# Optimization experiments

Hardware: AMD Instinct MI355X
Metric: run time of the kernel (lower is better)

The kernel has to match this reference:

```python
import jax, jax.numpy as jnp
import numpy as np

EMBED_DIM = 1024
ATTN_DIM = 256
B, NQ, NK = 16, 1, 4096


def setup_inputs() -> dict:
    key = jax.random.key(0)
    ks = jax.random.split(key, 7)
    return {
        "q": jax.random.normal(ks[0], (B, NQ, EMBED_DIM), dtype=jnp.float32),
        "k": jax.random.normal(ks[1], (B, NK, EMBED_DIM), dtype=jnp.float32),
        "v": jax.random.normal(ks[2], (B, NK, EMBED_DIM), dtype=jnp.float32),
        "W_kq": jax.random.normal(ks[3], (EMBED_DIM, ATTN_DIM), dtype=jnp.float32) * (1.0 / np.sqrt(EMBED_DIM)),
        "b_kq": jax.random.normal(ks[4], (ATTN_DIM,), dtype=jnp.float32) * 0.02,
        "W_v": jax.random.normal(ks[5], (EMBED_DIM, EMBED_DIM), dtype=jnp.float32) * (1.0 / np.sqrt(EMBED_DIM)),
        "b_v": jax.random.normal(ks[6], (EMBED_DIM,), dtype=jnp.float32) * 0.02,
    }


def reference(q, k, v, W_kq, b_kq, W_v, b_v):
    # Shared kq projection applied to both q and k (embedding_dim -> attention_dim)
    qp = jnp.einsum("bqd,da->bqa", q, W_kq) + b_kq          # [B, NQ, A]
    kp = jnp.einsum("bkd,da->bka", k, W_kq) + b_kq          # [B, NK, A]
    vp = jnp.einsum("bkd,de->bke", v, W_v) + b_v            # [B, NK, E]
    # scores = q @ k^T / sqrt(attention_dim)  (k.shape[2] after projection)
    scores = jnp.einsum("bqa,bka->bqk", qp, kp) / jnp.sqrt(
        jnp.asarray(kp.shape[2], dtype=qp.dtype))
    attn = jax.nn.softmax(scores, axis=2)                   # [B, NQ, NK]
    out = jnp.einsum("bqk,bke->bqe", attn, vp)              # [B, NQ, E]
    return out.squeeze(1)                                   # [B, E] since NQ == 1
```

## Files before the change

### kernel.cpp

```cpp
#include <hip/hip_runtime.h>

#define ED 1024
#define AD 256
#define BB 16
#define NK 4096
#define NCH 64
#define KCH (NK/NCH)

#define OFF_QP   0
#define OFF_T    4096
#define OFF_WSUM 20480
#define OFF_PART 21504
#define OFF_OV   1070080

__global__ void k_qp(const float* __restrict__ q, const float* __restrict__ Wkq,
                     const float* __restrict__ bkq, float* __restrict__ qp) {
    int b = blockIdx.x, cg = blockIdx.y, tid = threadIdx.x;
    int c = cg * 64 + (tid & 63), dg = tid >> 6;
    __shared__ float qsh[ED];
    ((float4*)qsh)[tid] = ((const float4*)(q + b * ED))[tid];
    __syncthreads();
    float acc = 0.f;
    #pragma unroll 8
    for (int d = dg; d < ED; d += 4) acc += qsh[d] * Wkq[(size_t)d * AD + c];
    __shared__ float red[4][64];
    red[dg][tid & 63] = acc;
    __syncthreads();
    if (tid < 64) {
        float s = red[0][tid] + red[1][tid] + red[2][tid] + red[3][tid];
        qp[b * AD + cg * 64 + tid] = s + bkq[cg * 64 + tid];
    }
}

__global__ void k_t(const float* __restrict__ Wkq, const float* __restrict__ qp,
                    float* __restrict__ t) {
    int b = blockIdx.y, dbase = blockIdx.x * 128;
    int tid = threadIdx.x, wave = tid >> 6, lane = tid & 63;
    float4 qv = ((const float4*)(qp + b * AD))[lane];
    for (int r = 0; r < 32; ++r) {
        int d = dbase + wave * 32 + r;
        float4 w = ((const float4*)(Wkq + (size_t)d * AD))[lane];
        float s = w.x * qv.x + w.y * qv.y + w.z * qv.z + w.w * qv.w;
        #pragma unroll
        for (int off = 32; off; off >>= 1) s += __shfl_down(s, off, 64);
        if (lane == 0) t[b * ED + d] = s;
    }
}

__global__ void k_fused(const float* __restrict__ k, const float* __restrict__ v,
                        const float* __restrict__ t, float* __restrict__ partial,
                        float* __restrict__ wsum) {
    int ch = blockIdx.x, b = blockIdx.y;
    int tid = threadIdx.x, wave = tid >> 6, lane = tid & 63;
    const float4* tb = (const float4*)(t + b * ED);
    float4 t0 = tb[lane], t1 = tb[64 + lane], t2 = tb[128 + lane], t3 = tb[192 + lane];
    __shared__ float ash[KCH];
    int row0 = ch * KCH + wave * 16;
    for (int r = 0; r < 16; ++r) {
        const float4* krow = (const float4*)(k + ((size_t)b * NK + row0 + r) * ED);
        float4 k0 = krow[lane], k1 = krow[64 + lane], k2 = krow[128 + lane], k3 = krow[192 + lane];
        float s = k0.x*t0.x + k0.y*t0.y + k0.z*t0.z + k0.w*t0.w
                + k1.x*t1.x + k1.y*t1.y + k1.z*t1.z + k1.w*t1.w
                + k2.x*t2.x + k2.y*t2.y + k2.z*t2.z + k2.w*t2.w
                + k3.x*t3.x + k3.y*t3.y + k3.z*t3.z + k3.w*t3.w;
        #pragma unroll
        for (int off = 32; off; off >>= 1) s += __shfl_down(s, off, 64);
        if (lane == 0) ash[wave * 16 + r] = __expf(s * 0.0625f);
    }
    __syncthreads();
    if (tid < KCH) {
        float s = ash[tid];
        #pragma unroll
        for (int off = 32; off; off >>= 1) s += __shfl_down(s, off, 64);
        if (tid == 0) wsum[b * NCH + ch] = s;
    }
    const float4* vb = (const float4*)(v + ((size_t)b * NK + (size_t)ch * KCH) * ED);
    float4 acc = {0.f, 0.f, 0.f, 0.f};
    #pragma unroll 4
    for (int kk = 0; kk < KCH; ++kk) {
        float wt = ash[kk];
        float4 vv = vb[(size_t)kk * (ED / 4) + tid];
        acc.x += wt * vv.x; acc.y += wt * vv.y; acc.z += wt * vv.z; acc.w += wt * vv.w;
    }
    ((float4*)partial)[((size_t)(b * NCH + ch)) * (ED / 4) + tid] = acc;
}

__global__ void k_reduce(const float* __restrict__ partial, const float* __restrict__ wsum,
                         float* __restrict__ ov) {
    int b = blockIdx.x, tid = threadIdx.x;
    __shared__ float lsh;
    if (tid < 64) {
        float s = wsum[b * NCH + tid];
        #pragma unroll
        for (int off = 32; off; off >>= 1) s += __shfl_down(s, off, 64);
        if (tid == 0) lsh = s;
    }
    __syncthreads();
    float linv = 1.0f / lsh;
    const float4* pb = (const float4*)(partial + (size_t)b * NCH * ED);
    float4 s4 = {0.f, 0.f, 0.f, 0.f};
    #pragma unroll 8
    for (int ch = 0; ch < NCH; ++ch) {
        float4 p = pb[(size_t)ch * (ED / 4) + tid];
        s4.x += p.x; s4.y += p.y; s4.z += p.z; s4.w += p.w;
    }
    s4.x *= linv; s4.y *= linv; s4.z *= linv; s4.w *= linv;
    ((float4*)(ov + b * ED))[tid] = s4;
}

__global__ void k_out(const float* __restrict__ ov, const float* __restrict__ Wv,
                      const float* __restrict__ bv, float* __restrict__ out) {
    int cb = blockIdx.x, tid = threadIdx.x;
    int col = cb * 64 + (tid & 63), dg = tid >> 6;
    __shared__ float ovsh[BB][ED];
    for (int i = tid; i < BB * ED / 4; i += 256)
        ((float4*)&ovsh[0][0])[i] = ((const float4*)ov)[i];
    __syncthreads();
    float acc[BB];
    #pragma unroll
    for (int b = 0; b < BB; ++b) acc[b] = 0.f;
    #pragma unroll 4
    for (int d = dg; d < ED; d += 4) {
        float w = Wv[(size_t)d * ED + col];
        #pragma unroll
        for (int b = 0; b < BB; ++b) acc[b] += ovsh[b][d] * w;
    }
    __shared__ float red[BB][256];
    #pragma unroll
    for (int b = 0; b < BB; ++b) red[b][tid] = acc[b];
    __syncthreads();
    #pragma unroll
    for (int bb = 0; bb < 4; ++bb) {
        int b = bb * 4 + (tid >> 6);
        int c = tid & 63;
        float s = red[b][c] + red[b][64 + c] + red[b][128 + c] + red[b][192 + c];
        out[b * ED + cb * 64 + c] = s + bv[cb * 64 + c];
    }
}

extern "C" void kernel_launch(void* const* d_in, const int* in_sizes, int n_in,
                              void* d_out, int out_size, void* d_ws, size_t ws_size,
                              hipStream_t stream) {
    const float* q   = (const float*)d_in[0];
    const float* k   = (const float*)d_in[1];
    const float* v   = (const float*)d_in[2];
    const float* Wkq = (const float*)d_in[3];
    const float* bkq = (const float*)d_in[4];
    const float* Wv  = (const float*)d_in[5];
    const float* bv  = (const float*)d_in[6];
    float* out = (float*)d_out;
    float* ws  = (float*)d_ws;

    float* qp      = ws + OFF_QP;
    float* t       = ws + OFF_T;
    float* wsum    = ws + OFF_WSUM;
    float* partial = ws + OFF_PART;
    float* ov      = ws + OFF_OV;

    k_qp    <<<dim3(16, 4),   256, 0, stream>>>(q, Wkq, bkq, qp);
    k_t     <<<dim3(8, 16),   256, 0, stream>>>(Wkq, qp, t);
    k_fused <<<dim3(NCH, BB), 256, 0, stream>>>(k, v, t, partial, wsum);
    k_reduce<<<16,            256, 0, stream>>>(partial, wsum, ov);
    k_out   <<<16,            256, 0, stream>>>(ov, Wv, bv, out);
}
```

Measured before the change: 208.4 us.

## Split reduce and output projection across more blocks, add final reduction kernel

Launches k_reduce and k_out on a 16x4 grid instead of 16 blocks, so each block handles one quarter of the embedding or reduction dimension. A new k_final kernel sums the four partial output projections and adds the bias. The change also processes two rows per iteration in k_t and k_fused for more memory-level parallelism, and raises the unroll factor of the V accumulation loop. The aim is to fill more compute units in the tail kernels, which were badly underoccupied. The cost is an extra kernel launch and an extra workspace round trip.

```diff
diff --git a/kernel.cpp b/kernel.cpp
--- a/kernel.cpp
+++ b/kernel.cpp
@@ -7,11 +7,12 @@
 #define NCH 64
 #define KCH (NK/NCH)
 
-#define OFF_QP   0
-#define OFF_T    4096
-#define OFF_WSUM 20480
-#define OFF_PART 21504
-#define OFF_OV   1070080
+#define OFF_QP    0
+#define OFF_T     4096
+#define OFF_WSUM  20480
+#define OFF_PART  21504
+#define OFF_OV    1070080
+#define OFF_OPART 1086464
 
 __global__ void k_qp(const float* __restrict__ q, const float* __restrict__ Wkq,
                      const float* __restrict__ bkq, float* __restrict__ qp) {
@@ -37,13 +38,19 @@
     int b = blockIdx.y, dbase = blockIdx.x * 128;
     int tid = threadIdx.x, wave = tid >> 6, lane = tid & 63;
     float4 qv = ((const float4*)(qp + b * AD))[lane];
-    for (int r = 0; r < 32; ++r) {
-        int d = dbase + wave * 32 + r;
-        float4 w = ((const float4*)(Wkq + (size_t)d * AD))[lane];
-        float s = w.x * qv.x + w.y * qv.y + w.z * qv.z + w.w * qv.w;
-        #pragma unroll
-        for (int off = 32; off; off >>= 1) s += __shfl_down(s, off, 64);
-        if (lane == 0) t[b * ED + d] = s;
+    for (int r = 0; r < 16; ++r) {
+        int d1 = dbase + wave * 32 + r;
+        int d2 = d1 + 16;
+        float4 w1 = ((const float4*)(Wkq + (size_t)d1 * AD))[lane];
+        float4 w2 = ((const float4*)(Wkq + (size_t)d2 * AD))[lane];
+        float s1 = w1.x*qv.x + w1.y*qv.y + w1.z*qv.z + w1.w*qv.w;
+        float s2 = w2.x*qv.x + w2.y*qv.y + w2.z*qv.z + w2.w*qv.w;
+        #pragma unroll
+        for (int off = 32; off; off >>= 1) {
+            s1 += __shfl_down(s1, off, 64);
+            s2 += __shfl_down(s2, off, 64);
+        }
+        if (lane == 0) { t[b * ED + d1] = s1; t[b * ED + d2] = s2; }
     }
 }
 
@@ -56,16 +63,28 @@
     float4 t0 = tb[lane], t1 = tb[64 + lane], t2 = tb[128 + lane], t3 = tb[192 + lane];
     __shared__ float ash[KCH];
     int row0 = ch * KCH + wave * 16;
-    for (int r = 0; r < 16; ++r) {
-        const float4* krow = (const float4*)(k + ((size_t)b * NK + row0 + r) * ED);
-        float4 k0 = krow[lane], k1 = krow[64 + lane], k2 = krow[128 + lane], k3 = krow[192 + lane];
-        float s = k0.x*t0.x + k0.y*t0.y + k0.z*t0.z + k0.w*t0.w
-                + k1.x*t1.x + k1.y*t1.y + k1.z*t1.z + k1.w*t1.w
-                + k2.x*t2.x + k2.y*t2.y + k2.z*t2.z + k2.w*t2.w
-                + k3.x*t3.x + k3.y*t3.y + k3.z*t3.z + k3.w*t3.w;
-        #pragma unroll
-        for (int off = 32; off; off >>= 1) s += __shfl_down(s, off, 64);
-        if (lane == 0) ash[wave * 16 + r] = __expf(s * 0.0625f);
+    for (int r = 0; r < 8; ++r) {
+        const float4* ka = (const float4*)(k + ((size_t)b * NK + row0 + r) * ED);
+        const float4* kb = (const float4*)(k + ((size_t)b * NK + row0 + r + 8) * ED);
+        float4 a0 = ka[lane], a1 = ka[64 + lane], a2 = ka[128 + lane], a3 = ka[192 + lane];
+        float4 b0 = kb[lane], b1 = kb[64 + lane], b2 = kb[128 + lane], b3 = kb[192 + lane];
+        float sa = a0.x*t0.x + a0.y*t0.y + a0.z*t0.z + a0.w*t0.w
+                 + a1.x*t1.x + a1.y*t1.y + a1.z*t1.z + a1.w*t1.w
+                 + a2.x*t2.x + a2.y*t2.y + a2.z*t2.z + a2.w*t2.w
+                 + a3.x*t3.x + a3.y*t3.y + a3.z*t3.z + a3.w*t3.w;
+        float sb = b0.x*t0.x + b0.y*t0.y + b0.z*t0.z + b0.w*t0.w
+                 + b1.x*t1.x + b1.y*t1.y + b1.z*t1.z + b1.w*t1.w
+                 + b2.x*t2.x + b2.y*t2.y + b2.z*t2.z + b2.w*t2.w
+                 + b3.x*t3.x + b3.y*t3.y + b3.z*t3.z + b3.w*t3.w;
+        #pragma unroll
+        for (int off = 32; off; off >>= 1) {
+            sa += __shfl_down(sa, off, 64);
+            sb += __shfl_down(sb, off, 64);
+        }
+        if (lane == 0) {
+            ash[wave * 16 + r]     = __expf(sa * 0.0625f);
+            ash[wave * 16 + r + 8] = __expf(sb * 0.0625f);
+        }
     }
     __syncthreads();
     if (tid < KCH) {
@@ -76,7 +95,7 @@
     }
     const float4* vb = (const float4*)(v + ((size_t)b * NK + (size_t)ch * KCH) * ED);
     float4 acc = {0.f, 0.f, 0.f, 0.f};
-    #pragma unroll 4
+    #pragma unroll 8
     for (int kk = 0; kk < KCH; ++kk) {
         float wt = ash[kk];
         float4 vv = vb[(size_t)kk * (ED / 4) + tid];
@@ -87,7 +106,8 @@
 
 __global__ void k_reduce(const float* __restrict__ partial, const float* __restrict__ wsum,
                          float* __restrict__ ov) {
-    int b = blockIdx.x, tid = threadIdx.x;
+    int b = blockIdx.x, dq = blockIdx.y, tid = threadIdx.x;
+    int chg = tid >> 6, c = tid & 63;
     __shared__ float lsh;
     if (tid < 64) {
         float s = wsum[b * NCH + tid];
@@ -95,47 +115,73 @@
         for (int off = 32; off; off >>= 1) s += __shfl_down(s, off, 64);
         if (tid == 0) lsh = s;
     }
-    __syncthreads();
-    float linv = 1.0f / lsh;
     const float4* pb = (const float4*)(partial + (size_t)b * NCH * ED);
     float4 s4 = {0.f, 0.f, 0.f, 0.f};
     #pragma unroll 8
-    for (int ch = 0; ch < NCH; ++ch) {
-        float4 p = pb[(size_t)ch * (ED / 4) + tid];
+    for (int ch = chg; ch < NCH; ch += 4) {
+        float4 p = pb[(size_t)ch * (ED / 4) + dq * 64 + c];
         s4.x += p.x; s4.y += p.y; s4.z += p.z; s4.w += p.w;
     }
-    s4.x *= linv; s4.y *= linv; s4.z *= linv; s4.w *= linv;
-    ((float4*)(ov + b * ED))[tid] = s4;
+    __shared__ float4 red[4][64];
+    red[chg][c] = s4;
+    __syncthreads();
+    if (tid < 64) {
+        float4 a0 = red[0][tid], a1 = red[1][tid], a2 = red[2][tid], a3 = red[3][tid];
+        float linv = 1.0f / lsh;
+        float4 r;
+        r.x = (a0.x + a1.x + a2.x + a3.x) * linv;
+        r.y = (a0.y + a1.y + a2.y + a3.y) * linv;
+        r.z = (a0.z + a1.z + a2.z + a3.z) * linv;
+        r.w = (a0.w + a1.w + a2.w + a3.w) * linv;
+        ((float4*)(ov + b * ED + dq * 256))[tid] = r;
+    }
 }
 
 __global__ void k_out(const float* __restrict__ ov, const float* __restrict__ Wv,
-                      const float* __restrict__ bv, float* __restrict__ out) {
-    int cb = blockIdx.x, tid = threadIdx.x;
+                      float* __restrict__ opart) {
+    int cb = blockIdx.x, dq = blockIdx.y, tid = threadIdx.x;
     int col = cb * 64 + (tid & 63), dg = tid >> 6;
-    __shared__ float ovsh[BB][ED];
-    for (int i = tid; i < BB * ED / 4; i += 256)
-        ((float4*)&ovsh[0][0])[i] = ((const float4*)ov)[i];
+    __shared__ float ovsh[BB][256];
+    for (int i = tid; i < BB * 64; i += 256) {
+        int bb = i >> 6, c4 = i & 63;
+        ((float4*)ovsh[bb])[c4] = ((const float4*)(ov + bb * ED + dq * 256))[c4];
+    }
     __syncthreads();
     float acc[BB];
     #pragma unroll
     for (int b = 0; b < BB; ++b) acc[b] = 0.f;
-    #pragma unroll 4
-    for (int d = dg; d < ED; d += 4) {
-        float w = Wv[(size_t)d * ED + col];
-        #pragma unroll
-        for (int b = 0; b < BB; ++b) acc[b] += ovsh[b][d] * w;
+    #pragma unroll 8
+    for (int it = 0; it < 64; ++it) {
+        int dd = dg + it * 4;
+        float w = Wv[(size_t)(dq * 256 + dd) * ED + col];
+        #pragma unroll
+        for (int b = 0; b < BB; ++b) acc[b] += ovsh[b][dd] * w;
     }
     __shared__ float red[BB][256];
     #pragma unroll
     for (int b = 0; b < BB; ++b) red[b][tid] = acc[b];
     __syncthreads();
-    #pragma unroll
-    for (int bb = 0; bb < 4; ++bb) {
-        int b = bb * 4 + (tid >> 6);
-        int c = tid & 63;
+    int bgrp = tid >> 6, c = tid & 63;
+    #pragma unroll
+    for (int bi = 0; bi < 4; ++bi) {
+        int b = bgrp * 4 + bi;
         float s = red[b][c] + red[b][64 + c] + red[b][128 + c] + red[b][192 + c];
-        out[b * ED + cb * 64 + c] = s + bv[cb * 64 + c];
-    }
+        opart[((size_t)(dq * BB + b)) * ED + cb * 64 + c] = s;
+    }
+}
+
+__global__ void k_final(const float* __restrict__ opart, const float* __restrict__ bv,
+                        float* __restrict__ out) {
+    int b = blockIdx.x, tid = threadIdx.x;
+    float4 s = ((const float4*)(opart + (size_t)(0 * BB + b) * ED))[tid];
+    #pragma unroll
+    for (int dq = 1; dq < 4; ++dq) {
+        float4 p = ((const float4*)(opart + (size_t)(dq * BB + b) * ED))[tid];
+        s.x += p.x; s.y += p.y; s.z += p.z; s.w += p.w;
+    }
+    float4 bb = ((const float4*)bv)[tid];
+    s.x += bb.x; s.y += bb.y; s.z += bb.z; s.w += bb.w;
+    ((float4*)(out + b * ED))[tid] = s;
 }
 
 extern "C" void kernel_launch(void* const* d_in, const int* in_sizes, int n_in,
@@ -156,10 +202,12 @@
     float* wsum    = ws + OFF_WSUM;
     float* partial = ws + OFF_PART;
     float* ov      = ws + OFF_OV;
+    float* opart   = ws + OFF_OPART;
 
     k_qp    <<<dim3(16, 4),   256, 0, stream>>>(q, Wkq, bkq, qp);
     k_t     <<<dim3(8, 16),   256, 0, stream>>>(Wkq, qp, t);
     k_fused <<<dim3(NCH, BB), 256, 0, stream>>>(k, v, t, partial, wsum);
-    k_reduce<<<16,            256, 0, stream>>>(partial, wsum, ov);
-    k_out   <<<16,            256, 0, stream>>>(ov, Wv, bv, out);
-}
+    k_reduce<<<dim3(16, 4),   256, 0, stream>>>(partial, wsum, ov);
+    k_out   <<<dim3(16, 4),   256, 0, stream>>>(ov, Wv, opart);
+    k_final <<<16,            256, 0, stream>>>(opart, bv, out);
+}
```

Result: faster. 175.3 us (-15.9%).
